# Kernel tuning notes

Hardware: AMD Instinct MI355X
Metric: run time of the kernel (lower is better)

## Reference

```python
import jax, jax.numpy as jnp
import numpy as np

BLOCK = 64  # block_size from config
NEG_INF = -1e9


def setup_inputs() -> dict:
    key = jax.random.key(0)
    k1, k2, k3, k4 = jax.random.split(key, 4)
    B, H, S, D = 2, 8, 2048, 64
    nb = S // BLOCK  # 32 blocks per side
    query = jax.random.normal(k1, (B, H, S, D), dtype=jnp.float32)
    key_t = jax.random.normal(k2, (B, H, S, D), dtype=jnp.float32)
    value = jax.random.normal(k3, (B, H, S, D), dtype=jnp.float32)
    # binary block mask; force diagonal blocks on so every row has >=1 valid key
    mat = jax.random.randint(k4, (nb, nb), 0, 2).astype(jnp.int32)
    mat = mat.at[jnp.arange(nb), jnp.arange(nb)].set(1)
    mask = jnp.ones((B, S), dtype=jnp.float32)  # padding mask (1 = keep)
    return {"query": query, "key": key_t, "value": value, "mask": mask, "mat": mat}


def reference(query, key, value, mask, mat):
    # Upsample block mask [nb, nb] -> dense [S, S] (nearest, like nn.Upsample)
    block_dense = jnp.repeat(jnp.repeat(mat, BLOCK, axis=0), BLOCK, axis=1) > 0
    # Block-sparse QK^T: only positions inside nonzero blocks participate.
    scores = jnp.einsum('bhqd,bhkd->bhqk', query, key)
    # Additive padding-mask bias, as in the original: 1e6 * (1 - mask)
    scores = scores - 1e6 * (1.0 - mask)[:, None, None, :]
    # Positions outside the block pattern are excluded from the softmax.
    scores = jnp.where(block_dense[None, None, :, :], scores, NEG_INF)
    attn = jax.nn.softmax(scores, axis=-1)
    out = jnp.einsum('bhqk,bhkd->bhqd', attn, value)
    return out
```

## Files before the change

kernel.cpp:

```cpp
#include <hip/hip_runtime.h>


typedef __attribute__((ext_vector_type(8))) short short8;
typedef __attribute__((ext_vector_type(4))) short short4_;
typedef __attribute__((ext_vector_type(4))) float float4_;
typedef __attribute__((ext_vector_type(8))) _Float16 half8_;

#define B_   2
#define H_   8
#define S_   2048
#define D_   64
#define NB_  32
#define KP   72
#define LOG2E 1.4426950408889634f

__device__ __forceinline__ short f2bf(float f) {
    union { float f; unsigned int u; } x; x.f = f;
    unsigned int r = x.u + 0x7FFFu + ((x.u >> 16) & 1u);
    return (short)(r >> 16);
}
__device__ __forceinline__ short f2bf_t(float f) {
    union { float f; unsigned int u; } x; x.f = f;
    return (short)(x.u >> 16);
}
__device__ __forceinline__ float bf2f(short s) {
    union { unsigned int u; float f; } x; x.u = ((unsigned int)(unsigned short)s) << 16;
    return x.f;
}
__device__ __forceinline__ short f2h(float f) {
    _Float16 h = (_Float16)f;
    return __builtin_bit_cast(short, h);
}
__device__ __forceinline__ int swz(int row, int gran) {
    return (row << 6) + (((gran ^ row) & 7) << 3);
}

__global__ __launch_bounds__(256)
void preconvert_kernel(const float* __restrict__ K, const float* __restrict__ V,
                       short* __restrict__ Khf, short* __restrict__ Vtb) {
    __shared__ short vn[64 * KP];
    const int tid = threadIdx.x;
    const int kt  = blockIdx.x;
    const int bh  = blockIdx.y;
    const size_t tb = ((size_t)bh * S_ + kt * 64) * D_;

#pragma unroll
    for (int it = 0; it < 4; ++it) {
        int i = tid + it * 256;
        int row = i >> 4, c4 = (i & 15) * 4;
        float4_ kv = *(const float4_*)(K + tb + row * D_ + c4);
        short4_ kh;
#pragma unroll
        for (int e = 0; e < 4; ++e) kh[e] = f2h(kv[e] * LOG2E);
        *(short4_*)(Khf + tb + row * D_ + c4) = kh;
        float4_ vv = *(const float4_*)(V + tb + row * D_ + c4);
        short4_ vb;
#pragma unroll
        for (int e = 0; e < 4; ++e) vb[e] = f2bf(vv[e]);
        *(short4_*)&vn[row * KP + c4] = vb;
    }
    __syncthreads();
#pragma unroll
    for (int it = 0; it < 2; ++it) {
        int i = tid + it * 256;
        int rowd = i >> 3, key8 = (i & 7) * 8;
        short8 o;
#pragma unroll
        for (int e = 0; e < 8; ++e) o[e] = vn[(key8 + e) * KP + rowd];
        *(short8*)(Vtb + (((size_t)(bh * NB_ + kt)) * 64 + rowd) * 64 + key8) = o;
    }
}

__global__ __launch_bounds__(128, 2)
void attn_mfma_db(const float* __restrict__ Q,
                  const float* __restrict__ Msk,
                  const int* __restrict__ Mat,
                  float* __restrict__ O,
                  const short* __restrict__ Khf_g,
                  const short* __restrict__ Vtb_g) {
    __shared__ __align__(16) short lds[4 * 4096 + 2 * 16 * KP];

    const int tid  = threadIdx.x;
    const int wave = tid >> 6;
    const int lane = tid & 63;
    const int c    = lane & 15;
    const int quad = lane >> 4;

    const int qt = blockIdx.x;
    const int bh = blockIdx.y;
    const int b  = bh / H_;
    const int qb = qt >> 1;
    const size_t base = (size_t)bh * S_ * D_;

    half8_ qa0, qa1;
    {
        const float* qp = Q + base + (size_t)(qt * 32 + wave * 16 + c) * D_ + quad * 8;
#pragma unroll
        for (int e = 0; e < 8; ++e) {
            qa0[e] = (_Float16)qp[e];
            qa1[e] = (_Float16)qp[e + 32];
        }
    }

    float4_ o[4];
    float l_part[4];
#pragma unroll
    for (int t = 0; t < 4; ++t) { o[t][0] = 0.f; o[t][1] = 0.f; o[t][2] = 0.f; o[t][3] = 0.f; }
#pragma unroll
    for (int j = 0; j < 4; ++j) l_part[j] = 0.f;

    unsigned long long bmv = __ballot(Mat[qb * NB_ + (lane & 31)] != 0);
    unsigned int mbits = (unsigned int)(bmv & 0xFFFFFFFFull);

    int srow[4], sgrn[4], soff[4];
#pragma unroll
    for (int it = 0; it < 4; ++it) {
        int i = tid + it * 128;
        srow[it] = i >> 3;
        sgrn[it] = i & 7;
        soff[it] = swz(srow[it], sgrn[it]);
    }
    int foff_lo[4], foff_hi[4];
#pragma unroll
    for (int t = 0; t < 4; ++t) {
        foff_lo[t] = swz(t * 16 + c, quad);
        foff_hi[t] = swz(t * 16 + c, quad + 4);
    }

    short8 sK[4], sV[4];
    float  biasn[4];

    int kb = __builtin_ctz(mbits);
    mbits &= mbits - 1;
    {
        const short* kh = Khf_g + base + (size_t)kb * 64 * D_;
        const short* vt = Vtb_g + ((size_t)(bh * NB_ + kb)) * 64 * 64;
#pragma unroll
        for (int it = 0; it < 4; ++it) {
            sK[it] = *(const short8*)(kh + srow[it] * 64 + sgrn[it] * 8);
            sV[it] = *(const short8*)(vt + srow[it] * 64 + sgrn[it] * 8);
        }
#pragma unroll
        for (int t = 0; t < 4; ++t)
            biasn[t] = -1.0e6f * LOG2E * (1.0f - Msk[(size_t)b * S_ + kb * 64 + t * 16 + c]);
#pragma unroll
        for (int it = 0; it < 4; ++it) {
            *(short8*)&lds[soff[it]]        = sK[it];
            *(short8*)&lds[8192 + soff[it]] = sV[it];
        }
    }
    __syncthreads();

    int pbo = 0;
    for (;;) {
        float biasc[4];
#pragma unroll
        for (int t = 0; t < 4; ++t) biasc[t] = biasn[t];

        const bool have_next = (mbits != 0);
        if (have_next) {
            kb = __builtin_ctz(mbits);
            mbits &= mbits - 1;
            const short* kh = Khf_g + base + (size_t)kb * 64 * D_;
            const short* vt = Vtb_g + ((size_t)(bh * NB_ + kb)) * 64 * 64;
#pragma unroll
            for (int it = 0; it < 4; ++it) {
                sK[it] = *(const short8*)(kh + srow[it] * 64 + sgrn[it] * 8);
                sV[it] = *(const short8*)(vt + srow[it] * 64 + sgrn[it] * 8);
            }
#pragma unroll
            for (int t = 0; t < 4; ++t)
                biasn[t] = -1.0e6f * LOG2E * (1.0f - Msk[(size_t)b * S_ + kb * 64 + t * 16 + c]);
        }

        float4_ sc[4];
#pragma unroll
        for (int t = 0; t < 4; ++t) { sc[t][0] = 0.f; sc[t][1] = 0.f; sc[t][2] = 0.f; sc[t][3] = 0.f; }
#pragma unroll
        for (int t = 0; t < 4; ++t) {
            half8_ kb0 = __builtin_bit_cast(half8_, *(const short8*)&lds[pbo + foff_lo[t]]);
            half8_ kb1 = __builtin_bit_cast(half8_, *(const short8*)&lds[pbo + foff_hi[t]]);
            sc[t] = __builtin_amdgcn_mfma_f32_16x16x32_f16(qa0, kb0, sc[t], 0, 0, 0);
            sc[t] = __builtin_amdgcn_mfma_f32_16x16x32_f16(qa1, kb1, sc[t], 0, 0, 0);
        }

        const int pwoff = 16384 + wave * 16 * KP;
#pragma unroll
        for (int t = 0; t < 4; ++t) {
#pragma unroll
            for (int j = 0; j < 4; ++j) {
                float p = exp2f(sc[t][j] + biasc[t]);
                l_part[j] += p;
                lds[pwoff + (quad * 4 + j) * KP + t * 16 + c] = f2bf_t(p);
            }
        }

        const short* pp = &lds[pwoff + c * KP + quad * 8];
        short8 pa0 = *(const short8*)(pp);
        short8 pa1 = *(const short8*)(pp + 32);

#pragma unroll
        for (int t = 0; t < 4; ++t) {
            short8 vb0 = *(const short8*)&lds[8192 + pbo + foff_lo[t]];
            short8 vb1 = *(const short8*)&lds[8192 + pbo + foff_hi[t]];
            o[t] = __builtin_amdgcn_mfma_f32_16x16x32_bf16(pa0, vb0, o[t], 0, 0, 0);
            o[t] = __builtin_amdgcn_mfma_f32_16x16x32_bf16(pa1, vb1, o[t], 0, 0, 0);
        }

        if (!have_next) break;

        const int nbo = pbo ^ 4096;
#pragma unroll
        for (int it = 0; it < 4; ++it) {
            *(short8*)&lds[nbo + soff[it]]        = sK[it];
            *(short8*)&lds[8192 + nbo + soff[it]] = sV[it];
        }
        __syncthreads();
        pbo = nbo;
    }

#pragma unroll
    for (int j = 0; j < 4; ++j) {
        float rs = l_part[j];
        rs += __shfl_xor(rs, 1);
        rs += __shfl_xor(rs, 2);
        rs += __shfl_xor(rs, 4);
        rs += __shfl_xor(rs, 8);
        float inv = 1.0f / rs;
        size_t rowoff = base + (size_t)(qt * 32 + wave * 16 + quad * 4 + j) * D_;
#pragma unroll
        for (int t = 0; t < 4; ++t)
            O[rowoff + t * 16 + c] = o[t][j] * inv;
    }
}

__global__ __launch_bounds__(256, 2)
void attn_mfma_fb(const float* __restrict__ Q,
                  const float* __restrict__ K,
                  const float* __restrict__ V,
                  const float* __restrict__ Msk,
                  const int* __restrict__ Mat,
                  float* __restrict__ O) {
    __shared__ __align__(16) short lds[4 * 64 * KP];
    short* Khi = lds;
    short* Klo = lds + 64 * KP;
    short* Vt  = lds + 2 * 64 * KP;
    short* Pl  = lds + 3 * 64 * KP;

    const int tid  = threadIdx.x;
    const int wave = tid >> 6;
    const int lane = tid & 63;
    const int c    = lane & 15;
    const int quad = lane >> 4;

    const int qb = blockIdx.x;
    const int bh = blockIdx.y;
    const int b  = bh / H_;
    const size_t base = (size_t)bh * S_ * D_;

    short8 qh0, qh1, ql0, ql1;
    {
        const float* qp = Q + base + (size_t)(qb * 64 + wave * 16 + c) * D_ + quad * 8;
#pragma unroll
        for (int e = 0; e < 8; ++e) {
            float f0 = qp[e], f1 = qp[e + 32];
            qh0[e] = f2bf(f0); ql0[e] = f2bf(f0 - bf2f(qh0[e]));
            qh1[e] = f2bf(f1); ql1[e] = f2bf(f1 - bf2f(qh1[e]));
        }
    }

    float4_ o[4];
    float l_part[4];
#pragma unroll
    for (int t = 0; t < 4; ++t) { o[t][0] = 0.f; o[t][1] = 0.f; o[t][2] = 0.f; o[t][3] = 0.f; }
#pragma unroll
    for (int j = 0; j < 4; ++j) l_part[j] = 0.f;

    for (int kb = 0; kb < NB_; ++kb) {
        if (Mat[qb * NB_ + kb] == 0) continue;

        __syncthreads();
        {
            const float* kg = K + base + (size_t)kb * 64 * D_;
            const float* vg = V + base + (size_t)kb * 64 * D_;
#pragma unroll
            for (int it = 0; it < 4; ++it) {
                int i = tid + it * 256;
                int row = i >> 4, c4 = (i & 15) * 4;
                float4_ kv = *(const float4_*)(kg + row * D_ + c4);
                short4_ hi, lo;
#pragma unroll
                for (int e = 0; e < 4; ++e) {
                    hi[e] = f2bf(kv[e]);
                    lo[e] = f2bf(kv[e] - bf2f(hi[e]));
                }
                *(short4_*)&Khi[row * KP + c4] = hi;
                *(short4_*)&Klo[row * KP + c4] = lo;
                float4_ vv = *(const float4_*)(vg + row * D_ + c4);
#pragma unroll
                for (int e = 0; e < 4; ++e) Vt[(c4 + e) * KP + row] = f2bf(vv[e]);
            }
        }
        __syncthreads();

        float4_ sc[4];
#pragma unroll
        for (int t = 0; t < 4; ++t) { sc[t][0] = 0.f; sc[t][1] = 0.f; sc[t][2] = 0.f; sc[t][3] = 0.f; }
#pragma unroll
        for (int t = 0; t < 4; ++t) {
            const short* kph = &Khi[(t * 16 + c) * KP + quad * 8];
            const short* kpl = &Klo[(t * 16 + c) * KP + quad * 8];
            short8 kh0 = *(const short8*)(kph);
            short8 kh1 = *(const short8*)(kph + 32);
            short8 kl0 = *(const short8*)(kpl);
            short8 kl1 = *(const short8*)(kpl + 32);
            sc[t] = __builtin_amdgcn_mfma_f32_16x16x32_bf16(qh0, kh0, sc[t], 0, 0, 0);
            sc[t] = __builtin_amdgcn_mfma_f32_16x16x32_bf16(qh1, kh1, sc[t], 0, 0, 0);
            sc[t] = __builtin_amdgcn_mfma_f32_16x16x32_bf16(qh0, kl0, sc[t], 0, 0, 0);
            sc[t] = __builtin_amdgcn_mfma_f32_16x16x32_bf16(qh1, kl1, sc[t], 0, 0, 0);
            sc[t] = __builtin_amdgcn_mfma_f32_16x16x32_bf16(ql0, kh0, sc[t], 0, 0, 0);
            sc[t] = __builtin_amdgcn_mfma_f32_16x16x32_bf16(ql1, kh1, sc[t], 0, 0, 0);
        }

        short* Pw = Pl + wave * 16 * KP;
#pragma unroll
        for (int t = 0; t < 4; ++t) {
            float bias = -1.0e6f * (1.0f - Msk[(size_t)b * S_ + kb * 64 + t * 16 + c]);
#pragma unroll
            for (int j = 0; j < 4; ++j) {
                float p = __expf(sc[t][j] + bias);
                l_part[j] += p;
                Pw[(quad * 4 + j) * KP + t * 16 + c] = f2bf(p);
            }
        }

        const short* pp = Pl + wave * 16 * KP + c * KP + quad * 8;
        short8 pa0 = *(const short8*)(pp);
        short8 pa1 = *(const short8*)(pp + 32);

#pragma unroll
        for (int t = 0; t < 4; ++t) {
            const short* vp = &Vt[(t * 16 + c) * KP + quad * 8];
            short8 vb0 = *(const short8*)(vp);
            short8 vb1 = *(const short8*)(vp + 32);
            o[t] = __builtin_amdgcn_mfma_f32_16x16x32_bf16(pa0, vb0, o[t], 0, 0, 0);
            o[t] = __builtin_amdgcn_mfma_f32_16x16x32_bf16(pa1, vb1, o[t], 0, 0, 0);
        }
    }

#pragma unroll
    for (int j = 0; j < 4; ++j) {
        float rs = l_part[j];
        rs += __shfl_xor(rs, 1);
        rs += __shfl_xor(rs, 2);
        rs += __shfl_xor(rs, 4);
        rs += __shfl_xor(rs, 8);
        float inv = 1.0f / rs;
        size_t rowoff = base + (size_t)(qb * 64 + wave * 16 + quad * 4 + j) * D_;
#pragma unroll
        for (int t = 0; t < 4; ++t)
            O[rowoff + t * 16 + c] = o[t][j] * inv;
    }
}

extern "C" void kernel_launch(void* const* d_in, const int* in_sizes, int n_in,
                              void* d_out, int out_size, void* d_ws, size_t ws_size,
                              hipStream_t stream) {
    const float* q   = (const float*)d_in[0];
    const float* k   = (const float*)d_in[1];
    const float* v   = (const float*)d_in[2];
    const float* msk = (const float*)d_in[3];
    const int*   mat = (const int*)d_in[4];
    float*       out = (float*)d_out;

    const size_t elems = (size_t)B_ * H_ * S_ * D_;
    const size_t need  = 2 * elems * sizeof(short);
    const int use_pre  = (ws_size >= need) ? 1 : 0;

    short* khf = (short*)d_ws;
    short* vtb = khf + elems;

    if (use_pre) {
        dim3 pgrid(NB_, B_ * H_);
        preconvert_kernel<<<pgrid, dim3(256), 0, stream>>>(k, v, khf, vtb);
        dim3 grid(S_ / 32, B_ * H_);
        attn_mfma_db<<<grid, dim3(128), 0, stream>>>(q, msk, mat, out, khf, vtb);
    } else {
        dim3 grid(NB_, B_ * H_);
        attn_mfma_fb<<<grid, dim3(256), 0, stream>>>(q, k, v, msk, mat, out);
    }
}
```

Baseline: 113.2 us.

## Process two key blocks per iteration instead of double-buffering single blocks

Restructures the main attention loop so each iteration handles a pair of active key blocks. The four LDS slots that previously held two double-buffered blocks now hold K and V for both blocks of the pair, and QK^T MFMAs for the two blocks are interleaved. This halves the number of loop iterations and barriers and gives more independent MFMA work per iteration. In exchange it drops the overlap between LDS staging and compute, since there are now two barriers per iteration around the store. It also doubles register staging, which may pressure occupancy, and an odd trailing block is computed anyway and masked out with a large negative bias.

```diff
diff --git a/kernel.cpp b/kernel.cpp
--- a/kernel.cpp
+++ b/kernel.cpp
@@ -72,12 +72,12 @@
 }
 
 __global__ __launch_bounds__(128, 2)
-void attn_mfma_db(const float* __restrict__ Q,
-                  const float* __restrict__ Msk,
-                  const int* __restrict__ Mat,
-                  float* __restrict__ O,
-                  const short* __restrict__ Khf_g,
-                  const short* __restrict__ Vtb_g) {
+void attn_mfma_pair(const float* __restrict__ Q,
+                    const float* __restrict__ Msk,
+                    const int* __restrict__ Mat,
+                    float* __restrict__ O,
+                    const short* __restrict__ Khf_g,
+                    const short* __restrict__ Vtb_g) {
     __shared__ __align__(16) short lds[4 * 4096 + 2 * 16 * KP];
 
     const int tid  = threadIdx.x;
@@ -127,96 +127,137 @@
         foff_hi[t] = swz(t * 16 + c, quad + 4);
     }
 
-    short8 sK[4], sV[4];
-    float  biasn[4];
-
-    int kb = __builtin_ctz(mbits);
-    mbits &= mbits - 1;
+    short8 sK[8], sV[8];
+    float  bias0n[4], bias1n[4];
+
+    int kb0 = __builtin_ctz(mbits); mbits &= mbits - 1;
+    int kb1; bool kill1;
+    if (mbits) { kb1 = __builtin_ctz(mbits); mbits &= mbits - 1; kill1 = false; }
+    else       { kb1 = kb0; kill1 = true; }
+
     {
-        const short* kh = Khf_g + base + (size_t)kb * 64 * D_;
-        const short* vt = Vtb_g + ((size_t)(bh * NB_ + kb)) * 64 * 64;
+        const short* kh0 = Khf_g + base + (size_t)kb0 * 64 * D_;
+        const short* vt0 = Vtb_g + ((size_t)(bh * NB_ + kb0)) * 64 * 64;
+        const short* kh1 = Khf_g + base + (size_t)kb1 * 64 * D_;
+        const short* vt1 = Vtb_g + ((size_t)(bh * NB_ + kb1)) * 64 * 64;
 #pragma unroll
         for (int it = 0; it < 4; ++it) {
-            sK[it] = *(const short8*)(kh + srow[it] * 64 + sgrn[it] * 8);
-            sV[it] = *(const short8*)(vt + srow[it] * 64 + sgrn[it] * 8);
-        }
-#pragma unroll
-        for (int t = 0; t < 4; ++t)
-            biasn[t] = -1.0e6f * LOG2E * (1.0f - Msk[(size_t)b * S_ + kb * 64 + t * 16 + c]);
+            sK[it]     = *(const short8*)(kh0 + srow[it] * 64 + sgrn[it] * 8);
+            sV[it]     = *(const short8*)(vt0 + srow[it] * 64 + sgrn[it] * 8);
+            sK[4 + it] = *(const short8*)(kh1 + srow[it] * 64 + sgrn[it] * 8);
+            sV[4 + it] = *(const short8*)(vt1 + srow[it] * 64 + sgrn[it] * 8);
+        }
+#pragma unroll
+        for (int t = 0; t < 4; ++t) {
+            bias0n[t] = -1.0e6f * LOG2E * (1.0f - Msk[(size_t)b * S_ + kb0 * 64 + t * 16 + c]);
+            bias1n[t] = kill1 ? -2.0e6f
+                              : -1.0e6f * LOG2E * (1.0f - Msk[(size_t)b * S_ + kb1 * 64 + t * 16 + c]);
+        }
+    }
+
+    for (;;) {
+        __syncthreads();
 #pragma unroll
         for (int it = 0; it < 4; ++it) {
-            *(short8*)&lds[soff[it]]        = sK[it];
-            *(short8*)&lds[8192 + soff[it]] = sV[it];
-        }
-    }
-    __syncthreads();
-
-    int pbo = 0;
-    for (;;) {
-        float biasc[4];
-#pragma unroll
-        for (int t = 0; t < 4; ++t) biasc[t] = biasn[t];
+            *(short8*)&lds[soff[it]]         = sK[it];
+            *(short8*)&lds[4096 + soff[it]]  = sK[4 + it];
+            *(short8*)&lds[8192 + soff[it]]  = sV[it];
+            *(short8*)&lds[12288 + soff[it]] = sV[4 + it];
+        }
+        float bias0c[4], bias1c[4];
+#pragma unroll
+        for (int t = 0; t < 4; ++t) { bias0c[t] = bias0n[t]; bias1c[t] = bias1n[t]; }
+        __syncthreads();
 
         const bool have_next = (mbits != 0);
         if (have_next) {
-            kb = __builtin_ctz(mbits);
-            mbits &= mbits - 1;
-            const short* kh = Khf_g + base + (size_t)kb * 64 * D_;
-            const short* vt = Vtb_g + ((size_t)(bh * NB_ + kb)) * 64 * 64;
+            kb0 = __builtin_ctz(mbits); mbits &= mbits - 1;
+            if (mbits) { kb1 = __builtin_ctz(mbits); mbits &= mbits - 1; kill1 = false; }
+            else       { kb1 = kb0; kill1 = true; }
+            const short* kh0 = Khf_g + base + (size_t)kb0 * 64 * D_;
+            const short* vt0 = Vtb_g + ((size_t)(bh * NB_ + kb0)) * 64 * 64;
+            const short* kh1 = Khf_g + base + (size_t)kb1 * 64 * D_;
+            const short* vt1 = Vtb_g + ((size_t)(bh * NB_ + kb1)) * 64 * 64;
 #pragma unroll
             for (int it = 0; it < 4; ++it) {
-                sK[it] = *(const short8*)(kh + srow[it] * 64 + sgrn[it] * 8);
-                sV[it] = *(const short8*)(vt + srow[it] * 64 + sgrn[it] * 8);
-            }
-#pragma unroll
-            for (int t = 0; t < 4; ++t)
-                biasn[t] = -1.0e6f * LOG2E * (1.0f - Msk[(size_t)b * S_ + kb * 64 + t * 16 + c]);
-        }
-
-        float4_ sc[4];
-#pragma unroll
-        for (int t = 0; t < 4; ++t) { sc[t][0] = 0.f; sc[t][1] = 0.f; sc[t][2] = 0.f; sc[t][3] = 0.f; }
-#pragma unroll
-        for (int t = 0; t < 4; ++t) {
-            half8_ kb0 = __builtin_bit_cast(half8_, *(const short8*)&lds[pbo + foff_lo[t]]);
-            half8_ kb1 = __builtin_bit_cast(half8_, *(const short8*)&lds[pbo + foff_hi[t]]);
-            sc[t] = __builtin_amdgcn_mfma_f32_16x16x32_f16(qa0, kb0, sc[t], 0, 0, 0);
-            sc[t] = __builtin_amdgcn_mfma_f32_16x16x32_f16(qa1, kb1, sc[t], 0, 0, 0);
+                sK[it]     = *(const short8*)(kh0 + srow[it] * 64 + sgrn[it] * 8);
+                sV[it]     = *(const short8*)(vt0 + srow[it] * 64 + sgrn[it] * 8);
+                sK[4 + it] = *(const short8*)(kh1 + srow[it] * 64 + sgrn[it] * 8);
+                sV[4 + it] = *(const short8*)(vt1 + srow[it] * 64 + sgrn[it] * 8);
+            }
+#pragma unroll
+            for (int t = 0; t < 4; ++t) {
+                bias0n[t] = -1.0e6f * LOG2E * (1.0f - Msk[(size_t)b * S_ + kb0 * 64 + t * 16 + c]);
+                bias1n[t] = kill1 ? -2.0e6f
+                                  : -1.0e6f * LOG2E * (1.0f - Msk[(size_t)b * S_ + kb1 * 64 + t * 16 + c]);
+            }
+        }
+
+        float4_ sc0[4], sc1[4];
+#pragma unroll
+        for (int t = 0; t < 4; ++t) {
+            sc0[t][0] = 0.f; sc0[t][1] = 0.f; sc0[t][2] = 0.f; sc0[t][3] = 0.f;
+            sc1[t][0] = 0.f; sc1[t][1] = 0.f; sc1[t][2] = 0.f; sc1[t][3] = 0.f;
+        }
+#pragma unroll
+        for (int t = 0; t < 4; ++t) {
+            half8_ a0 = __builtin_bit_cast(half8_, *(const short8*)&lds[foff_lo[t]]);
+            half8_ a1 = __builtin_bit_cast(half8_, *(const short8*)&lds[foff_hi[t]]);
+            half8_ b0 = __builtin_bit_cast(half8_, *(const short8*)&lds[4096 + foff_lo[t]]);
+            half8_ b1 = __builtin_bit_cast(half8_, *(const short8*)&lds[4096 + foff_hi[t]]);
+            sc0[t] = __builtin_amdgcn_mfma_f32_16x16x32_f16(qa0, a0, sc0[t], 0, 0, 0);
+            sc1[t] = __builtin_amdgcn_mfma_f32_16x16x32_f16(qa0, b0, sc1[t], 0, 0, 0);
+            sc0[t] = __builtin_amdgcn_mfma_f32_16x16x32_f16(qa1, a1, sc0[t], 0, 0, 0);
+            sc1[t] = __builtin_amdgcn_mfma_f32_16x16x32_f16(qa1, b1, sc1[t], 0, 0, 0);
         }
 
         const int pwoff = 16384 + wave * 16 * KP;
+
 #pragma unroll
         for (int t = 0; t < 4; ++t) {
 #pragma unroll
             for (int j = 0; j < 4; ++j) {
-                float p = exp2f(sc[t][j] + biasc[t]);
+                float p = exp2f(sc0[t][j] + bias0c[t]);
                 l_part[j] += p;
                 lds[pwoff + (quad * 4 + j) * KP + t * 16 + c] = f2bf_t(p);
             }
         }
-
-        const short* pp = &lds[pwoff + c * KP + quad * 8];
-        short8 pa0 = *(const short8*)(pp);
-        short8 pa1 = *(const short8*)(pp + 32);
-
-#pragma unroll
-        for (int t = 0; t < 4; ++t) {
-            short8 vb0 = *(const short8*)&lds[8192 + pbo + foff_lo[t]];
-            short8 vb1 = *(const short8*)&lds[8192 + pbo + foff_hi[t]];
-            o[t] = __builtin_amdgcn_mfma_f32_16x16x32_bf16(pa0, vb0, o[t], 0, 0, 0);
-            o[t] = __builtin_amdgcn_mfma_f32_16x16x32_bf16(pa1, vb1, o[t], 0, 0, 0);
+        {
+            const short* pp = &lds[pwoff + c * KP + quad * 8];
+            short8 pa0 = *(const short8*)(pp);
+            short8 pa1 = *(const short8*)(pp + 32);
+#pragma unroll
+            for (int t = 0; t < 4; ++t) {
+                short8 vb0 = *(const short8*)&lds[8192 + foff_lo[t]];
+                short8 vb1 = *(const short8*)&lds[8192 + foff_hi[t]];
+                o[t] = __builtin_amdgcn_mfma_f32_16x16x32_bf16(pa0, vb0, o[t], 0, 0, 0);
+                o[t] = __builtin_amdgcn_mfma_f32_16x16x32_bf16(pa1, vb1, o[t], 0, 0, 0);
+            }
+        }
+
+#pragma unroll
+        for (int t = 0; t < 4; ++t) {
+#pragma unroll
+            for (int j = 0; j < 4; ++j) {
+                float p = exp2f(sc1[t][j] + bias1c[t]);
+                l_part[j] += p;
+                lds[pwoff + (quad * 4 + j) * KP + t * 16 + c] = f2bf_t(p);
+            }
+        }
+        {
+            const short* pp = &lds[pwoff + c * KP + quad * 8];
+            short8 pa0 = *(const short8*)(pp);
+            short8 pa1 = *(const short8*)(pp + 32);
+#pragma unroll
+            for (int t = 0; t < 4; ++t) {
+                short8 vb0 = *(const short8*)&lds[12288 + foff_lo[t]];
+                short8 vb1 = *(const short8*)&lds[12288 + foff_hi[t]];
+                o[t] = __builtin_amdgcn_mfma_f32_16x16x32_bf16(pa0, vb0, o[t], 0, 0, 0);
+                o[t] = __builtin_amdgcn_mfma_f32_16x16x32_bf16(pa1, vb1, o[t], 0, 0, 0);
+            }
         }
 
         if (!have_next) break;
-
-        const int nbo = pbo ^ 4096;
-#pragma unroll
-        for (int it = 0; it < 4; ++it) {
-            *(short8*)&lds[nbo + soff[it]]        = sK[it];
-            *(short8*)&lds[8192 + nbo + soff[it]] = sV[it];
-        }
-        __syncthreads();
-        pbo = nbo;
     }
 
 #pragma unroll
@@ -384,7 +425,7 @@
         dim3 pgrid(NB_, B_ * H_);
         preconvert_kernel<<<pgrid, dim3(256), 0, stream>>>(k, v, khf, vtb);
         dim3 grid(S_ / 32, B_ * H_);
-        attn_mfma_db<<<grid, dim3(128), 0, stream>>>(q, msk, mat, out, khf, vtb);
+        attn_mfma_pair<<<grid, dim3(128), 0, stream>>>(q, msk, mat, out, khf, vtb);
     } else {
         dim3 grid(NB_, B_ * H_);
         attn_mfma_fb<<<grid, dim3(256), 0, stream>>>(q, k, v, msk, mat, out);
```

New measurement: 117.4 us. 1.04x slower.

## Split key blocks across two workgroups per query tile and add combine pass

Applied to the files above, without the earlier changes.

Replaces the 32-row, 128-thread double-buffered attention kernel with a 64-row, 256-thread kernel. Each query tile's nonzero key blocks are split across two workgroups by alternating index, and each writes unnormalized partial outputs and row sums. A new combine kernel adds the two partials and normalizes. The split aims to shorten per-workgroup serial work, but adds a third launch, extra global traffic for the partials, and drops the LDS double buffering in favour of two barriers per iteration. Skipping the running max is safe because the two halves share one reference frame.

```diff
diff --git a/kernel.cpp b/kernel.cpp
--- a/kernel.cpp
+++ b/kernel.cpp
@@ -71,14 +71,15 @@
     }
 }
 
-__global__ __launch_bounds__(128, 2)
-void attn_mfma_db(const float* __restrict__ Q,
-                  const float* __restrict__ Msk,
-                  const int* __restrict__ Mat,
-                  float* __restrict__ O,
-                  const short* __restrict__ Khf_g,
-                  const short* __restrict__ Vtb_g) {
-    __shared__ __align__(16) short lds[4 * 4096 + 2 * 16 * KP];
+__global__ __launch_bounds__(256, 2)
+void attn_ks(const float* __restrict__ Q,
+             const float* __restrict__ Msk,
+             const int* __restrict__ Mat,
+             float* __restrict__ Opart,
+             float* __restrict__ Lpart,
+             const short* __restrict__ Khf_g,
+             const short* __restrict__ Vtb_g) {
+    __shared__ __align__(16) short lds[8192 + 4 * 16 * KP];
 
     const int tid  = threadIdx.x;
     const int wave = tid >> 6;
@@ -86,15 +87,16 @@
     const int c    = lane & 15;
     const int quad = lane >> 4;
 
-    const int qt = blockIdx.x;
-    const int bh = blockIdx.y;
-    const int b  = bh / H_;
-    const int qb = qt >> 1;
+    const int qb   = blockIdx.x;
+    const int bh   = blockIdx.y;
+    const int half = blockIdx.z;
+    const int b    = bh / H_;
     const size_t base = (size_t)bh * S_ * D_;
+    const size_t NOUT = (size_t)B_ * H_ * S_ * D_;
 
     half8_ qa0, qa1;
     {
-        const float* qp = Q + base + (size_t)(qt * 32 + wave * 16 + c) * D_ + quad * 8;
+        const float* qp = Q + base + (size_t)(qb * 64 + wave * 16 + c) * D_ + quad * 8;
 #pragma unroll
         for (int e = 0; e < 8; ++e) {
             qa0[e] = (_Float16)qp[e];
@@ -110,12 +112,21 @@
     for (int j = 0; j < 4; ++j) l_part[j] = 0.f;
 
     unsigned long long bmv = __ballot(Mat[qb * NB_ + (lane & 31)] != 0);
-    unsigned int mbits = (unsigned int)(bmv & 0xFFFFFFFFull);
-
-    int srow[4], sgrn[4], soff[4];
-#pragma unroll
-    for (int it = 0; it < 4; ++it) {
-        int i = tid + it * 128;
+    unsigned int mb = (unsigned int)(bmv & 0xFFFFFFFFull);
+    unsigned int mine = 0;
+    {
+        unsigned int t = mb; int idx = 0;
+        while (t) {
+            int k = __builtin_ctz(t); t &= t - 1;
+            if ((idx & 1) == half) mine |= (1u << k);
+            ++idx;
+        }
+    }
+
+    int srow[2], sgrn[2], soff[2];
+#pragma unroll
+    for (int it = 0; it < 2; ++it) {
+        int i = tid + it * 256;
         srow[it] = i >> 3;
         sgrn[it] = i & 7;
         soff[it] = swz(srow[it], sgrn[it]);
@@ -127,44 +138,15 @@
         foff_hi[t] = swz(t * 16 + c, quad + 4);
     }
 
-    short8 sK[4], sV[4];
-    float  biasn[4];
-
-    int kb = __builtin_ctz(mbits);
-    mbits &= mbits - 1;
-    {
-        const short* kh = Khf_g + base + (size_t)kb * 64 * D_;
-        const short* vt = Vtb_g + ((size_t)(bh * NB_ + kb)) * 64 * 64;
-#pragma unroll
-        for (int it = 0; it < 4; ++it) {
-            sK[it] = *(const short8*)(kh + srow[it] * 64 + sgrn[it] * 8);
-            sV[it] = *(const short8*)(vt + srow[it] * 64 + sgrn[it] * 8);
-        }
-#pragma unroll
-        for (int t = 0; t < 4; ++t)
-            biasn[t] = -1.0e6f * LOG2E * (1.0f - Msk[(size_t)b * S_ + kb * 64 + t * 16 + c]);
-#pragma unroll
-        for (int it = 0; it < 4; ++it) {
-            *(short8*)&lds[soff[it]]        = sK[it];
-            *(short8*)&lds[8192 + soff[it]] = sV[it];
-        }
-    }
-    __syncthreads();
-
-    int pbo = 0;
-    for (;;) {
-        float biasc[4];
-#pragma unroll
-        for (int t = 0; t < 4; ++t) biasc[t] = biasn[t];
-
-        const bool have_next = (mbits != 0);
-        if (have_next) {
-            kb = __builtin_ctz(mbits);
-            mbits &= mbits - 1;
+    if (mine) {
+        short8 sK[2], sV[2];
+        float  biasn[4];
+        int kb = __builtin_ctz(mine); mine &= mine - 1;
+        {
             const short* kh = Khf_g + base + (size_t)kb * 64 * D_;
             const short* vt = Vtb_g + ((size_t)(bh * NB_ + kb)) * 64 * 64;
 #pragma unroll
-            for (int it = 0; it < 4; ++it) {
+            for (int it = 0; it < 2; ++it) {
                 sK[it] = *(const short8*)(kh + srow[it] * 64 + sgrn[it] * 8);
                 sV[it] = *(const short8*)(vt + srow[it] * 64 + sgrn[it] * 8);
             }
@@ -173,50 +155,69 @@
                 biasn[t] = -1.0e6f * LOG2E * (1.0f - Msk[(size_t)b * S_ + kb * 64 + t * 16 + c]);
         }
 
-        float4_ sc[4];
-#pragma unroll
-        for (int t = 0; t < 4; ++t) { sc[t][0] = 0.f; sc[t][1] = 0.f; sc[t][2] = 0.f; sc[t][3] = 0.f; }
-#pragma unroll
-        for (int t = 0; t < 4; ++t) {
-            half8_ kb0 = __builtin_bit_cast(half8_, *(const short8*)&lds[pbo + foff_lo[t]]);
-            half8_ kb1 = __builtin_bit_cast(half8_, *(const short8*)&lds[pbo + foff_hi[t]]);
-            sc[t] = __builtin_amdgcn_mfma_f32_16x16x32_f16(qa0, kb0, sc[t], 0, 0, 0);
-            sc[t] = __builtin_amdgcn_mfma_f32_16x16x32_f16(qa1, kb1, sc[t], 0, 0, 0);
-        }
-
-        const int pwoff = 16384 + wave * 16 * KP;
-#pragma unroll
-        for (int t = 0; t < 4; ++t) {
-#pragma unroll
-            for (int j = 0; j < 4; ++j) {
-                float p = exp2f(sc[t][j] + biasc[t]);
-                l_part[j] += p;
-                lds[pwoff + (quad * 4 + j) * KP + t * 16 + c] = f2bf_t(p);
-            }
-        }
-
-        const short* pp = &lds[pwoff + c * KP + quad * 8];
-        short8 pa0 = *(const short8*)(pp);
-        short8 pa1 = *(const short8*)(pp + 32);
-
-#pragma unroll
-        for (int t = 0; t < 4; ++t) {
-            short8 vb0 = *(const short8*)&lds[8192 + pbo + foff_lo[t]];
-            short8 vb1 = *(const short8*)&lds[8192 + pbo + foff_hi[t]];
-            o[t] = __builtin_amdgcn_mfma_f32_16x16x32_bf16(pa0, vb0, o[t], 0, 0, 0);
-            o[t] = __builtin_amdgcn_mfma_f32_16x16x32_bf16(pa1, vb1, o[t], 0, 0, 0);
-        }
-
-        if (!have_next) break;
-
-        const int nbo = pbo ^ 4096;
-#pragma unroll
-        for (int it = 0; it < 4; ++it) {
-            *(short8*)&lds[nbo + soff[it]]        = sK[it];
-            *(short8*)&lds[8192 + nbo + soff[it]] = sV[it];
-        }
-        __syncthreads();
-        pbo = nbo;
+        for (;;) {
+            __syncthreads();
+#pragma unroll
+            for (int it = 0; it < 2; ++it) {
+                *(short8*)&lds[soff[it]]        = sK[it];
+                *(short8*)&lds[4096 + soff[it]] = sV[it];
+            }
+            float biasc[4];
+#pragma unroll
+            for (int t = 0; t < 4; ++t) biasc[t] = biasn[t];
+            __syncthreads();
+
+            const bool have_next = (mine != 0);
+            if (have_next) {
+                kb = __builtin_ctz(mine); mine &= mine - 1;
+                const short* kh = Khf_g + base + (size_t)kb * 64 * D_;
+                const short* vt = Vtb_g + ((size_t)(bh * NB_ + kb)) * 64 * 64;
+#pragma unroll
+                for (int it = 0; it < 2; ++it) {
+                    sK[it] = *(const short8*)(kh + srow[it] * 64 + sgrn[it] * 8);
+                    sV[it] = *(const short8*)(vt + srow[it] * 64 + sgrn[it] * 8);
+                }
+#pragma unroll
+                for (int t = 0; t < 4; ++t)
+                    biasn[t] = -1.0e6f * LOG2E * (1.0f - Msk[(size_t)b * S_ + kb * 64 + t * 16 + c]);
+            }
+
+            float4_ sc[4];
+#pragma unroll
+            for (int t = 0; t < 4; ++t) { sc[t][0] = 0.f; sc[t][1] = 0.f; sc[t][2] = 0.f; sc[t][3] = 0.f; }
+#pragma unroll
+            for (int t = 0; t < 4; ++t) {
+                half8_ kb0 = __builtin_bit_cast(half8_, *(const short8*)&lds[foff_lo[t]]);
+                half8_ kb1 = __builtin_bit_cast(half8_, *(const short8*)&lds[foff_hi[t]]);
+                sc[t] = __builtin_amdgcn_mfma_f32_16x16x32_f16(qa0, kb0, sc[t], 0, 0, 0);
+                sc[t] = __builtin_amdgcn_mfma_f32_16x16x32_f16(qa1, kb1, sc[t], 0, 0, 0);
+            }
+
+            const int pwoff = 8192 + wave * 16 * KP;
+#pragma unroll
+            for (int t = 0; t < 4; ++t) {
+#pragma unroll
+                for (int j = 0; j < 4; ++j) {
+                    float p = exp2f(sc[t][j] + biasc[t]);
+                    l_part[j] += p;
+                    lds[pwoff + (quad * 4 + j) * KP + t * 16 + c] = f2bf_t(p);
+                }
+            }
+
+            const short* pp = &lds[pwoff + c * KP + quad * 8];
+            short8 pa0 = *(const short8*)(pp);
+            short8 pa1 = *(const short8*)(pp + 32);
+
+#pragma unroll
+            for (int t = 0; t < 4; ++t) {
+                short8 vb0 = *(const short8*)&lds[4096 + foff_lo[t]];
+                short8 vb1 = *(const short8*)&lds[4096 + foff_hi[t]];
+                o[t] = __builtin_amdgcn_mfma_f32_16x16x32_bf16(pa0, vb0, o[t], 0, 0, 0);
+                o[t] = __builtin_amdgcn_mfma_f32_16x16x32_bf16(pa1, vb1, o[t], 0, 0, 0);
+            }
+
+            if (!have_next) break;
+        }
     }
 
 #pragma unroll
@@ -226,12 +227,32 @@
         rs += __shfl_xor(rs, 2);
         rs += __shfl_xor(rs, 4);
         rs += __shfl_xor(rs, 8);
-        float inv = 1.0f / rs;
-        size_t rowoff = base + (size_t)(qt * 32 + wave * 16 + quad * 4 + j) * D_;
+        const int srow_ = qb * 64 + wave * 16 + quad * 4 + j;
+        float* Op = Opart + (size_t)half * NOUT + base + (size_t)srow_ * D_;
 #pragma unroll
         for (int t = 0; t < 4; ++t)
-            O[rowoff + t * 16 + c] = o[t][j] * inv;
-    }
+            Op[t * 16 + c] = o[t][j];
+        if (c == 0)
+            Lpart[(size_t)half * (B_ * H_ * S_) + (size_t)bh * S_ + srow_] = rs;
+    }
+}
+
+__global__ __launch_bounds__(256)
+void combine_kernel(const float* __restrict__ Opart,
+                    const float* __restrict__ Lpart,
+                    float* __restrict__ O) {
+    const size_t N = (size_t)B_ * H_ * S_ * D_;
+    size_t i = ((size_t)blockIdx.x * 256 + threadIdx.x) * 4;
+    if (i >= N) return;
+    int row = (int)(i >> 6);
+    float4_ a = *(const float4_*)(Opart + i);
+    float4_ bq = *(const float4_*)(Opart + N + i);
+    float l = Lpart[row] + Lpart[(size_t)B_ * H_ * S_ + row];
+    float inv = 1.0f / l;
+    float4_ r;
+    r[0] = (a[0] + bq[0]) * inv; r[1] = (a[1] + bq[1]) * inv;
+    r[2] = (a[2] + bq[2]) * inv; r[3] = (a[3] + bq[3]) * inv;
+    *(float4_*)(O + i) = r;
 }
 
 __global__ __launch_bounds__(256, 2)
@@ -374,17 +395,22 @@
     float*       out = (float*)d_out;
 
     const size_t elems = (size_t)B_ * H_ * S_ * D_;
-    const size_t need  = 2 * elems * sizeof(short);
+    const size_t need  = 2 * elems * sizeof(short)
+                       + 2 * elems * sizeof(float)
+                       + 2 * (size_t)B_ * H_ * S_ * sizeof(float);
     const int use_pre  = (ws_size >= need) ? 1 : 0;
 
-    short* khf = (short*)d_ws;
-    short* vtb = khf + elems;
+    short* khf   = (short*)d_ws;
+    short* vtb   = khf + elems;
+    float* opart = (float*)(vtb + elems);
+    float* lpart = opart + 2 * elems;
 
     if (use_pre) {
         dim3 pgrid(NB_, B_ * H_);
         preconvert_kernel<<<pgrid, dim3(256), 0, stream>>>(k, v, khf, vtb);
-        dim3 grid(S_ / 32, B_ * H_);
-        attn_mfma_db<<<grid, dim3(128), 0, stream>>>(q, msk, mat, out, khf, vtb);
+        dim3 grid(NB_, B_ * H_, 2);
+        attn_ks<<<grid, dim3(256), 0, stream>>>(q, msk, mat, opart, lpart, khf, vtb);
+        combine_kernel<<<dim3((unsigned)(elems / 4 / 256)), dim3(256), 0, stream>>>(opart, lpart, out);
     } else {
         dim3 grid(NB_, B_ * H_);
         attn_mfma_fb<<<grid, dim3(256), 0, stream>>>(q, k, v, msk, mat, out);
```

Measured after the change: 110.6 us. 2.3% less time.

## Split key blocks across two wave groups per 64-row query tile and merge partials

Applied to the files above, without the earlier changes.

Replaces the 128-thread, 32-row-per-block kernel with a 512-thread kernel that covers a whole 64-row query block. Its eight waves form two halves, and each half processes alternating active key blocks with its own LDS K/V buffer. The two partial outputs and row sums are merged through LDS at the end. This shares the Q tile and block mask across more waves and halves the serial key-block chain per wave. In exchange it drops the previous double-buffered prefetch overlap, adds two barriers per iteration plus a final reduction, and runs dummy iterations when the count of active blocks is odd.

```diff
diff --git a/kernel.cpp b/kernel.cpp
--- a/kernel.cpp
+++ b/kernel.cpp
@@ -71,30 +71,35 @@
     }
 }
 
-__global__ __launch_bounds__(128, 2)
-void attn_mfma_db(const float* __restrict__ Q,
-                  const float* __restrict__ Msk,
-                  const int* __restrict__ Mat,
-                  float* __restrict__ O,
-                  const short* __restrict__ Khf_g,
-                  const short* __restrict__ Vtb_g) {
-    __shared__ __align__(16) short lds[4 * 4096 + 2 * 16 * KP];
+__global__ __launch_bounds__(512, 4)
+void attn_fused(const float* __restrict__ Q,
+                const float* __restrict__ Msk,
+                const int* __restrict__ Mat,
+                float* __restrict__ O,
+                const short* __restrict__ Khf_g,
+                const short* __restrict__ Vtb_g) {
+    __shared__ __align__(16) short lds[16384 + 8 * 16 * KP];
 
     const int tid  = threadIdx.x;
     const int wave = tid >> 6;
+    const int half = wave >> 2;
+    const int qtw  = wave & 3;
     const int lane = tid & 63;
     const int c    = lane & 15;
     const int quad = lane >> 4;
-
-    const int qt = blockIdx.x;
+    const int hid  = tid & 255;
+
+    const int qb = blockIdx.x;
     const int bh = blockIdx.y;
     const int b  = bh / H_;
-    const int qb = qt >> 1;
     const size_t base = (size_t)bh * S_ * D_;
+
+    const int hbK = half * 4096;
+    const int hbV = 8192 + half * 4096;
 
     half8_ qa0, qa1;
     {
-        const float* qp = Q + base + (size_t)(qt * 32 + wave * 16 + c) * D_ + quad * 8;
+        const float* qp = Q + base + (size_t)(qb * 64 + qtw * 16 + c) * D_ + quad * 8;
 #pragma unroll
         for (int e = 0; e < 8; ++e) {
             qa0[e] = (_Float16)qp[e];
@@ -110,12 +115,23 @@
     for (int j = 0; j < 4; ++j) l_part[j] = 0.f;
 
     unsigned long long bmv = __ballot(Mat[qb * NB_ + (lane & 31)] != 0);
-    unsigned int mbits = (unsigned int)(bmv & 0xFFFFFFFFull);
-
-    int srow[4], sgrn[4], soff[4];
-#pragma unroll
-    for (int it = 0; it < 4; ++it) {
-        int i = tid + it * 128;
+    unsigned int mb = (unsigned int)(bmv & 0xFFFFFFFFull);
+    const int nact  = __popc(mb);
+    const int niter = (nact + 1) >> 1;
+    unsigned int mine = 0;
+    {
+        unsigned int tb2 = mb; int idx = 0;
+        while (tb2) {
+            int k = __builtin_ctz(tb2); tb2 &= tb2 - 1;
+            if ((idx & 1) == half) mine |= (1u << k);
+            ++idx;
+        }
+    }
+
+    int srow[2], sgrn[2], soff[2];
+#pragma unroll
+    for (int it = 0; it < 2; ++it) {
+        int i = hid + it * 256;
         srow[it] = i >> 3;
         sgrn[it] = i & 7;
         soff[it] = swz(srow[it], sgrn[it]);
@@ -127,50 +143,55 @@
         foff_hi[t] = swz(t * 16 + c, quad + 4);
     }
 
-    short8 sK[4], sV[4];
+    short8 sK[2], sV[2];
     float  biasn[4];
-
-    int kb = __builtin_ctz(mbits);
-    mbits &= mbits - 1;
+    int kb; bool kill;
+    if (mine) { kb = __builtin_ctz(mine); mine &= mine - 1; kill = false; }
+    else      { kb = __builtin_ctz(mb); kill = true; }
     {
         const short* kh = Khf_g + base + (size_t)kb * 64 * D_;
         const short* vt = Vtb_g + ((size_t)(bh * NB_ + kb)) * 64 * 64;
 #pragma unroll
-        for (int it = 0; it < 4; ++it) {
+        for (int it = 0; it < 2; ++it) {
             sK[it] = *(const short8*)(kh + srow[it] * 64 + sgrn[it] * 8);
             sV[it] = *(const short8*)(vt + srow[it] * 64 + sgrn[it] * 8);
         }
 #pragma unroll
         for (int t = 0; t < 4; ++t)
-            biasn[t] = -1.0e6f * LOG2E * (1.0f - Msk[(size_t)b * S_ + kb * 64 + t * 16 + c]);
-#pragma unroll
-        for (int it = 0; it < 4; ++it) {
-            *(short8*)&lds[soff[it]]        = sK[it];
-            *(short8*)&lds[8192 + soff[it]] = sV[it];
-        }
-    }
-    __syncthreads();
-
-    int pbo = 0;
-    for (;;) {
+            biasn[t] = kill ? -2.0e6f
+                            : -1.0e6f * LOG2E * (1.0f - Msk[(size_t)b * S_ + kb * 64 + t * 16 + c]);
+    }
+
+    for (int it2 = 0; it2 < niter; ++it2) {
+        __syncthreads();
+#pragma unroll
+        for (int s = 0; s < 2; ++s) {
+            *(short8*)&lds[hbK + soff[s]] = sK[s];
+            *(short8*)&lds[hbV + soff[s]] = sV[s];
+        }
         float biasc[4];
 #pragma unroll
         for (int t = 0; t < 4; ++t) biasc[t] = biasn[t];
-
-        const bool have_next = (mbits != 0);
-        if (have_next) {
-            kb = __builtin_ctz(mbits);
-            mbits &= mbits - 1;
-            const short* kh = Khf_g + base + (size_t)kb * 64 * D_;
-            const short* vt = Vtb_g + ((size_t)(bh * NB_ + kb)) * 64 * 64;
-#pragma unroll
-            for (int it = 0; it < 4; ++it) {
-                sK[it] = *(const short8*)(kh + srow[it] * 64 + sgrn[it] * 8);
-                sV[it] = *(const short8*)(vt + srow[it] * 64 + sgrn[it] * 8);
+        __syncthreads();
+
+        if (it2 + 1 < niter) {
+            if (mine) { kb = __builtin_ctz(mine); mine &= mine - 1; kill = false; }
+            else      { kill = true; }
+            if (!kill) {
+                const short* kh = Khf_g + base + (size_t)kb * 64 * D_;
+                const short* vt = Vtb_g + ((size_t)(bh * NB_ + kb)) * 64 * 64;
+#pragma unroll
+                for (int s = 0; s < 2; ++s) {
+                    sK[s] = *(const short8*)(kh + srow[s] * 64 + sgrn[s] * 8);
+                    sV[s] = *(const short8*)(vt + srow[s] * 64 + sgrn[s] * 8);
+                }
+#pragma unroll
+                for (int t = 0; t < 4; ++t)
+                    biasn[t] = -1.0e6f * LOG2E * (1.0f - Msk[(size_t)b * S_ + kb * 64 + t * 16 + c]);
+            } else {
+#pragma unroll
+                for (int t = 0; t < 4; ++t) biasn[t] = -2.0e6f;
             }
-#pragma unroll
-            for (int t = 0; t < 4; ++t)
-                biasn[t] = -1.0e6f * LOG2E * (1.0f - Msk[(size_t)b * S_ + kb * 64 + t * 16 + c]);
         }
 
         float4_ sc[4];
@@ -178,8 +199,8 @@
         for (int t = 0; t < 4; ++t) { sc[t][0] = 0.f; sc[t][1] = 0.f; sc[t][2] = 0.f; sc[t][3] = 0.f; }
 #pragma unroll
         for (int t = 0; t < 4; ++t) {
-            half8_ kb0 = __builtin_bit_cast(half8_, *(const short8*)&lds[pbo + foff_lo[t]]);
-            half8_ kb1 = __builtin_bit_cast(half8_, *(const short8*)&lds[pbo + foff_hi[t]]);
+            half8_ kb0 = __builtin_bit_cast(half8_, *(const short8*)&lds[hbK + foff_lo[t]]);
+            half8_ kb1 = __builtin_bit_cast(half8_, *(const short8*)&lds[hbK + foff_hi[t]]);
             sc[t] = __builtin_amdgcn_mfma_f32_16x16x32_f16(qa0, kb0, sc[t], 0, 0, 0);
             sc[t] = __builtin_amdgcn_mfma_f32_16x16x32_f16(qa1, kb1, sc[t], 0, 0, 0);
         }
@@ -201,36 +222,40 @@
 
 #pragma unroll
         for (int t = 0; t < 4; ++t) {
-            short8 vb0 = *(const short8*)&lds[8192 + pbo + foff_lo[t]];
-            short8 vb1 = *(const short8*)&lds[8192 + pbo + foff_hi[t]];
+            short8 vb0 = *(const short8*)&lds[hbV + foff_lo[t]];
+            short8 vb1 = *(const short8*)&lds[hbV + foff_hi[t]];
             o[t] = __builtin_amdgcn_mfma_f32_16x16x32_bf16(pa0, vb0, o[t], 0, 0, 0);
             o[t] = __builtin_amdgcn_mfma_f32_16x16x32_bf16(pa1, vb1, o[t], 0, 0, 0);
         }
-
-        if (!have_next) break;
-
-        const int nbo = pbo ^ 4096;
-#pragma unroll
-        for (int it = 0; it < 4; ++it) {
-            *(short8*)&lds[nbo + soff[it]]        = sK[it];
-            *(short8*)&lds[8192 + nbo + soff[it]] = sV[it];
-        }
-        __syncthreads();
-        pbo = nbo;
-    }
-
-#pragma unroll
-    for (int j = 0; j < 4; ++j) {
-        float rs = l_part[j];
-        rs += __shfl_xor(rs, 1);
-        rs += __shfl_xor(rs, 2);
-        rs += __shfl_xor(rs, 4);
-        rs += __shfl_xor(rs, 8);
-        float inv = 1.0f / rs;
-        size_t rowoff = base + (size_t)(qt * 32 + wave * 16 + quad * 4 + j) * D_;
+    }
+
+    __syncthreads();
+    float* fl = (float*)lds;
+    if (half == 1) {
+        const int idx = ((wave - 4) * 64 + lane) * 21;
 #pragma unroll
         for (int t = 0; t < 4; ++t)
-            O[rowoff + t * 16 + c] = o[t][j] * inv;
+#pragma unroll
+            for (int j = 0; j < 4; ++j) fl[idx + t * 4 + j] = o[t][j];
+#pragma unroll
+        for (int j = 0; j < 4; ++j) fl[idx + 16 + j] = l_part[j];
+    }
+    __syncthreads();
+    if (half == 0) {
+        const int idx = (wave * 64 + lane) * 21;
+#pragma unroll
+        for (int j = 0; j < 4; ++j) {
+            float rs = l_part[j] + fl[idx + 16 + j];
+            rs += __shfl_xor(rs, 1);
+            rs += __shfl_xor(rs, 2);
+            rs += __shfl_xor(rs, 4);
+            rs += __shfl_xor(rs, 8);
+            float inv = 1.0f / rs;
+            size_t rowoff = base + (size_t)(qb * 64 + qtw * 16 + quad * 4 + j) * D_;
+#pragma unroll
+            for (int t = 0; t < 4; ++t)
+                O[rowoff + t * 16 + c] = (o[t][j] + fl[idx + t * 4 + j]) * inv;
+        }
     }
 }
 
@@ -383,8 +408,8 @@
     if (use_pre) {
         dim3 pgrid(NB_, B_ * H_);
         preconvert_kernel<<<pgrid, dim3(256), 0, stream>>>(k, v, khf, vtb);
-        dim3 grid(S_ / 32, B_ * H_);
-        attn_mfma_db<<<grid, dim3(128), 0, stream>>>(q, msk, mat, out, khf, vtb);
+        dim3 grid(NB_, B_ * H_);
+        attn_fused<<<grid, dim3(512), 0, stream>>>(q, msk, mat, out, khf, vtb);
     } else {
         dim3 grid(NB_, B_ * H_);
         attn_mfma_fb<<<grid, dim3(256), 0, stream>>>(q, k, v, msk, mat, out);
```

Result: faster. 107.8 us (-4.7%).
